# Performance work log

Hardware: AMD Instinct MI355X
Metric: run time of the kernel (lower is better)

The kernel has to match this reference:

```python
import jax, jax.numpy as jnp
from jax import lax
import numpy as np

ND1, ND2 = 48, 8   # stage_configs
LAMB = 1.5
EPS = 1e-12


def _make_proj(scale, n_views):
    H, W = 512 // scale, 640 // scale
    f = 700.0 / scale
    K = np.array([[f, 0, W / 2], [0, f, H / 2], [0, 0, 1]], np.float32)
    mats = []
    for v in range(n_views):
        a = 0.04 * v
        R = np.array([[np.cos(a), 0, np.sin(a)], [0, 1, 0], [-np.sin(a), 0, np.cos(a)]], np.float32)
        E = np.eye(4, dtype=np.float32)
        E[:3, :3] = R
        E[0, 3] = 20.0 * v
        Kin = np.eye(4, dtype=np.float32)
        Kin[:3, :3] = K
        mats.append(np.stack([E, Kin]))
    return jnp.asarray(np.stack(mats))[None]  # [1,V,2,4,4]


def setup_inputs():
    key = jax.random.key(0)
    ks = jax.random.split(key, 5)
    return {
        'feats1': jax.random.normal(ks[0], (1, 3, 32, 128, 160), jnp.float32),
        'feats2': jax.random.normal(ks[1], (1, 3, 16, 256, 320), jnp.float32),
        'proj1': _make_proj(4, 3),
        'proj2': _make_proj(2, 3),
        'depth_values': jnp.linspace(425.0, 935.0, ND1, dtype=jnp.float32)[None],
        'img': jax.random.normal(ks[2], (1, 3, 512, 640), jnp.float32),
        'w1': jax.random.normal(ks[3], (1, 32, 3, 3, 3), jnp.float32) * 0.05,
        'b1': jnp.zeros((1,), jnp.float32),
        'w2': jax.random.normal(ks[4], (1, 16, 3, 3, 3), jnp.float32) * 0.05,
        'b2': jnp.zeros((1,), jnp.float32),
    }


def _compose(p):
    # p: [B,2,4,4] -> K @ E[:3,:4] placed in top 3 rows of the extrinsic
    top = jnp.einsum('bij,bjk->bik', p[:, 1, :3, :3], p[:, 0, :3, :4])
    return p[:, 0].at[:, :3, :4].set(top)


def _bilinear(fea, x, y):
    # grid_sample(mode='bilinear', padding_mode='zeros', align_corners=False)
    # fea [B,C,H,W]; x,y pixel coords [B,P] -> [B,C,P]
    B, C, H, W = fea.shape
    flat = fea.reshape(B, C, H * W)
    x0, y0 = jnp.floor(x), jnp.floor(y)

    def gather(xi, yi):
        valid = (xi >= 0) & (xi <= W - 1) & (yi >= 0) & (yi <= H - 1)
        idx = (jnp.clip(yi, 0, H - 1) * W + jnp.clip(xi, 0, W - 1)).astype(jnp.int32)
        v = jnp.take_along_axis(flat, idx[:, None, :], axis=2)
        return jnp.where(valid[:, None, :], v, 0.0)

    wx, wy = x - x0, y - y0
    return (gather(x0, y0) * ((1 - wx) * (1 - wy))[:, None]
            + gather(x0 + 1, y0) * (wx * (1 - wy))[:, None]
            + gather(x0, y0 + 1) * ((1 - wx) * wy)[:, None]
            + gather(x0 + 1, y0 + 1) * (wx * wy)[:, None])


def _homo_warp(src_fea, src_proj, ref_proj, depth_samps):
    B, C, H, W = src_fea.shape
    D = depth_samps.shape[1]
    proj = jnp.einsum('bij,bjk->bik', src_proj, jnp.linalg.inv(ref_proj))
    rot, trans = proj[:, :3, :3], proj[:, :3, 3:4]
    yy, xx = jnp.meshgrid(jnp.arange(H, dtype=src_fea.dtype),
                          jnp.arange(W, dtype=src_fea.dtype), indexing='ij')
    xyz = jnp.stack([xx.ravel(), yy.ravel(), jnp.ones(H * W, src_fea.dtype)])  # [3,HW]
    rot_xyz = jnp.einsum('bij,jp->bip', rot, xyz)                               # [B,3,HW]
    pxyz = rot_xyz[:, :, None, :] * depth_samps.reshape(B, 1, D, -1) + trans[:, :, None, :]  # [B,3,D,HW]
    gx = pxyz[:, 0] / pxyz[:, 2] / ((W - 1) / 2) - 1.0
    gy = pxyz[:, 1] / pxyz[:, 2] / ((H - 1) / 2) - 1.0
    ix = ((gx + 1.0) * W - 1.0) / 2.0  # unnormalize, align_corners=False
    iy = ((gy + 1.0) * H - 1.0) / 2.0
    warped = _bilinear(src_fea, ix.reshape(B, -1), iy.reshape(B, -1))
    return warped.reshape(B, C, D, H, W)


def _conv3d(x, w, b):
    y = lax.conv_general_dilated(x, w, (1, 1, 1), 'SAME',
                                 dimension_numbers=('NCDHW', 'OIDHW', 'NCDHW'))
    return y + b.reshape(1, -1, 1, 1, 1)


def _stage(feats, projs, depth_samps, w, b):
    # feats [B,V,C,H,W], projs [B,V,2,4,4], depth_samps [B,D,H,W]
    B, V, C, H, W = feats.shape
    D = depth_samps.shape[1]
    ref_proj = _compose(projs[:, 0])
    ref_vol = jnp.broadcast_to(feats[:, 0][:, :, None], (B, C, D, H, W))
    vsum, vsq = ref_vol, ref_vol ** 2
    for v in range(1, V):  # small fixed number of views
        wv = _homo_warp(feats[:, v], _compose(projs[:, v]), ref_proj, depth_samps)
        vsum = vsum + wv
        vsq = vsq + wv ** 2
    variance = vsq / V - (vsum / V) ** 2
    prob = jax.nn.softmax(_conv3d(variance, w, b)[:, 0], axis=1)  # [B,D,H,W]
    depth = jnp.sum(prob * depth_samps, axis=1)                   # [B,H,W]
    p = jnp.pad(prob, ((0, 0), (1, 2), (0, 0), (0, 0)))
    sum4 = p[:, 0:D] + p[:, 1:D + 1] + p[:, 2:D + 2] + p[:, 3:D + 3]  # 4*avg_pool3d((4,1,1))
    di = jnp.sum(prob * jnp.arange(D, dtype=prob.dtype)[None, :, None, None], axis=1)
    di = jnp.clip(di.astype(jnp.int32), 0, D - 1)
    conf = jnp.take_along_axis(sum4, di[:, None], axis=1)[:, 0]
    exp_var = LAMB * jnp.sqrt(jnp.sum((depth_samps - depth[:, None]) ** 2 * prob, axis=1))
    return depth, conf, exp_var


def _forward(feats1, feats2, proj1, proj2, depth_values, img, w1, b1, w2, b2):
    B, _, Hi, Wi = img.shape
    H1, W1 = Hi // 4, Wi // 4
    H2, W2 = Hi // 2, Wi // 2
    # stage 1: depth_values is [B,D] -> uniform sampling path
    dmin, dmax = depth_values[:, 0], depth_values[:, -1]
    step1 = (dmax - dmin) / (ND1 - 1)
    s1 = dmin[:, None] + jnp.arange(ND1, dtype=jnp.float32)[None] * step1[:, None]
    samps1 = jnp.broadcast_to(s1[:, :, None, None], (B, ND1, H1, W1))
    d1, c1, v1 = _stage(feats1, proj1, samps1, w1, b1)
    # stage 2: detach + bilinear upsample + uncertainty-aware samples
    cur_d = jax.image.resize(lax.stop_gradient(d1)[:, None], (B, 1, H2, W2), 'bilinear')
    cur_v = jax.image.resize(lax.stop_gradient(v1)[:, None], (B, 1, H2, W2), 'bilinear')
    low = -jnp.minimum(cur_d, cur_v)
    step2 = (cur_v - low) / (ND2 - 1.0)
    samps2 = cur_d + low + step2 * jnp.arange(ND2, dtype=jnp.float32)[None, :, None, None] + EPS
    d2, c2, v2 = _stage(feats2, proj2, samps2, w2, b2)
    return (d1, c1, v1, d2, c2, v2)


def reference(feats1, feats2, proj1, proj2, depth_values, img, w1, b1, w2, b2):
    return _forward(feats1, feats2, proj1, proj2, depth_values, img, w1, b1, w2, b2)
```

## Files before the change

### kernel.cpp

```cpp
#include <hip/hip_runtime.h>
#include <math.h>


typedef _Float16 half2_t __attribute__((ext_vector_type(2)));
typedef _Float16 half8_t __attribute__((ext_vector_type(8)));

union U4H { uint4 u; half2_t h[4]; };
union U2H { uint2 u; half2_t h[2]; };

static __device__ inline float fdot2f(half2_t a, half2_t b, float c) {
#if __has_builtin(__builtin_amdgcn_fdot2)
  return __builtin_amdgcn_fdot2(a, b, c, false);
#else
  return c + (float)a[0] * (float)b[0] + (float)a[1] * (float)b[1];
#endif
}

__global__ void setup_mats_kernel(const float* __restrict__ proj1,
                                  const float* __restrict__ proj2,
                                  const float* __restrict__ depthv, int nd,
                                  float* __restrict__ ws,
                                  const float* __restrict__ w1,
                                  const float* __restrict__ w2,
                                  _Float16* __restrict__ w2a,
                                  _Float16* __restrict__ w2b) {
  const int tid = threadIdx.x;
  if (w2a != nullptr) {
    for (int i = tid; i < 27 * 32; i += 256) {
      int c = i % 32, r = i / 32, kd = r % 3, t = r / 3;
      w2a[(t * 3 + kd) * 32 + c] = (_Float16)w1[c * 27 + kd * 9 + t];
    }
    for (int i = tid; i < 27 * 16; i += 256) {
      int c = i % 16, r = i / 16, kd = r % 3, t = r / 3;
      w2b[(t * 3 + kd) * 16 + c] = (_Float16)w2[c * 27 + kd * 9 + t];
    }
  }
  if (tid != 0) return;
  for (int s = 0; s < 2; ++s) {
    const float* P = s ? proj2 : proj1;
    double comp[3][4][4];
    for (int v = 0; v < 3; ++v) {
      const float* E = P + v * 32;
      const float* K = P + v * 32 + 16;
      for (int r = 0; r < 3; ++r)
        for (int c = 0; c < 4; ++c) {
          double acc = 0.0;
          for (int k = 0; k < 3; ++k) acc += (double)K[r * 4 + k] * (double)E[k * 4 + c];
          comp[v][r][c] = acc;
        }
      for (int c = 0; c < 4; ++c) comp[v][3][c] = (double)E[12 + c];
    }
    double a[4][8];
    for (int r = 0; r < 4; ++r)
      for (int c = 0; c < 4; ++c) {
        a[r][c] = comp[0][r][c];
        a[r][4 + c] = (r == c) ? 1.0 : 0.0;
      }
    for (int col = 0; col < 4; ++col) {
      int piv = col;
      double best = fabs(a[col][col]);
      for (int r = col + 1; r < 4; ++r) {
        double t = fabs(a[r][col]);
        if (t > best) { best = t; piv = r; }
      }
      if (piv != col)
        for (int c = 0; c < 8; ++c) { double t = a[col][c]; a[col][c] = a[piv][c]; a[piv][c] = t; }
      double dv = a[col][col];
      for (int c = 0; c < 8; ++c) a[col][c] /= dv;
      for (int r = 0; r < 4; ++r)
        if (r != col) {
          double f = a[r][col];
          if (f != 0.0)
            for (int c = 0; c < 8; ++c) a[r][c] -= f * a[col][c];
        }
    }
    for (int v = 1; v < 3; ++v) {
      double Pm[3][4];
      for (int r = 0; r < 3; ++r)
        for (int c = 0; c < 4; ++c) {
          double acc = 0.0;
          for (int k = 0; k < 4; ++k) acc += comp[v][r][k] * a[k][4 + c];
          Pm[r][c] = acc;
        }
      float* o = ws + s * 24 + (v - 1) * 12;
      o[0] = (float)Pm[0][0]; o[1] = (float)Pm[0][1]; o[2] = (float)Pm[0][2];
      o[3] = (float)Pm[1][0]; o[4] = (float)Pm[1][1]; o[5] = (float)Pm[1][2];
      o[6] = (float)Pm[2][0]; o[7] = (float)Pm[2][1]; o[8] = (float)Pm[2][2];
      o[9] = (float)Pm[0][3]; o[10] = (float)Pm[1][3]; o[11] = (float)Pm[2][3];
    }
  }
  ws[48] = depthv[0];
  ws[49] = (depthv[nd - 1] - depthv[0]) / 47.0f;
}

template <int C, int H, int W>
__device__ inline void transpose_body(const float* __restrict__ in,
                                      _Float16* __restrict__ out,
                                      int x, int h, int v, float* s_t) {
  const int tid = threadIdx.x;
  const int w0 = x * 32;
  for (int r = tid; r < C * 32; r += 256) {
    int c = r >> 5, w = r & 31;
    s_t[c * 33 + w] = in[((size_t)(v * C + c) * H + h) * W + w0 + w];
  }
  __syncthreads();
  for (int r = tid; r < 32 * C; r += 256) {
    int w = r / C, c = r - (r / C) * C;
    out[((size_t)(v * H + h) * W + w0 + w) * C + c] = (_Float16)s_t[c * 33 + w];
  }
}

__global__ void transpose_both_kernel(const float* __restrict__ in1,
                                      _Float16* __restrict__ out1,
                                      const float* __restrict__ in2,
                                      _Float16* __restrict__ out2) {
  __shared__ float s_t[32 * 33];
  int bid = blockIdx.x;
  if (bid < 1920) {
    int x = bid % 5, h = (bid / 5) % 128, v = bid / (5 * 128);
    transpose_body<32, 128, 160>(in1, out1, x, h, v, s_t);
  } else {
    int b = bid - 1920;
    int x = b % 10, h = (b / 10) % 256, v = b / (10 * 256);
    transpose_body<16, 256, 320>(in2, out2, x, h, v, s_t);
  }
}

template <int D, int H, int W>
__device__ inline void stage2_range(const float* __restrict__ prev_d,
                                    const float* __restrict__ prev_v,
                                    int gy, int gx, float& base, float& st) {
  constexpr int SH = H / 2, SW = W / 2;
  float syf = 0.5f * (float)gy - 0.25f;
  float sxf = 0.5f * (float)gx - 0.25f;
  syf = fminf(fmaxf(syf, 0.0f), (float)(SH - 1));
  sxf = fminf(fmaxf(sxf, 0.0f), (float)(SW - 1));
  int sy0 = (int)syf, sx0 = (int)sxf;
  float fy2 = syf - (float)sy0, fx2 = sxf - (float)sx0;
  int sy1 = min(sy0 + 1, SH - 1), sx1 = min(sx0 + 1, SW - 1);
  int j00 = sy0 * SW + sx0, j01 = sy0 * SW + sx1;
  int j10 = sy1 * SW + sx0, j11 = sy1 * SW + sx1;
  float cd = (prev_d[j00] * (1.f - fx2) + prev_d[j01] * fx2) * (1.f - fy2) +
             (prev_d[j10] * (1.f - fx2) + prev_d[j11] * fx2) * fy2;
  float cv = (prev_v[j00] * (1.f - fx2) + prev_v[j01] * fx2) * (1.f - fy2) +
             (prev_v[j10] * (1.f - fx2) + prev_v[j11] * fx2) * fy2;
  float lo = -fminf(cd, cv);
  base = cd + lo + 1e-12f;
  st = (cv - lo) / (float)(D - 1);
}

template <int D, int H, int W>
__global__ void range_kernel(const float* __restrict__ prev_d,
                             const float* __restrict__ prev_v,
                             float2* __restrict__ rng) {
  int pix = blockIdx.x * 256 + threadIdx.x;
  if (pix >= H * W) return;
  float b, s;
  stage2_range<D, H, W>(prev_d, prev_v, pix / W, pix % W, b, s);
  rng[pix] = make_float2(b, s);
}

template <int C, int DTOT, int H, int W, bool STAGE2>
__launch_bounds__(256)
__global__ void gather_var_kernel(const _Float16* __restrict__ feats,
                                  const float* __restrict__ mats,
                                  const float* __restrict__ dpar,
                                  const float2* __restrict__ rng,
                                  _Float16* __restrict__ var_out) {
  constexpr int C8 = C / 8;
  const int idx = blockIdx.x * 256 + threadIdx.x;
  if (idx >= DTOT * H * W) return;
  const int gx = idx % W;
  const int t2 = idx / W;
  const int gy = t2 % H;
  const int d = t2 / H;
  const int pix = gy * W + gx;

  float base, st;
  if constexpr (STAGE2) {
    float2 r = rng[pix];
    base = r.x;
    st = r.y;
  } else {
    base = dpar[0];
    st = dpar[1];
  }
  const float dep = base + (float)d * st;

  const half8_t* fp = (const half8_t*)feats;
  float s[C], q[C];
#pragma unroll
  for (int cg = 0; cg < C8; ++cg) {
    half8_t r = fp[(size_t)pix * C8 + cg];
#pragma unroll
    for (int j = 0; j < 8; ++j) {
      float x = (float)r[j];
      s[cg * 8 + j] = x;
      q[cg * 8 + j] = x * x;
    }
  }

#pragma unroll
  for (int v = 0; v < 2; ++v) {
    const float* M = mats + v * 12;
    float fx = (float)gx, fy = (float)gy;
    float X = (M[0] * fx + M[1] * fy + M[2]) * dep + M[9];
    float Y = (M[3] * fx + M[4] * fy + M[5]) * dep + M[10];
    float Z = (M[6] * fx + M[7] * fy + M[8]) * dep + M[11];
    float inv = 1.0f / Z;
    float xz = X * inv, yz = Y * inv;
    float gxn = xz * (2.0f / (float)(W - 1)) - 1.0f;
    float gyn = yz * (2.0f / (float)(H - 1)) - 1.0f;
    float ix = ((gxn + 1.0f) * (float)W - 1.0f) * 0.5f;
    float iy = ((gyn + 1.0f) * (float)H - 1.0f) * 0.5f;
    float x0f = floorf(ix), y0f = floorf(iy);
    float wx = ix - x0f, wy = iy - y0f;
    float x1f = x0f + 1.0f, y1f = y0f + 1.0f;
    bool vx0 = (x0f >= 0.0f) && (x0f <= (float)(W - 1));
    bool vx1 = (x1f >= 0.0f) && (x1f <= (float)(W - 1));
    bool vy0 = (y0f >= 0.0f) && (y0f <= (float)(H - 1));
    bool vy1 = (y1f >= 0.0f) && (y1f <= (float)(H - 1));
    int xc0 = (int)fminf(fmaxf(x0f, 0.0f), (float)(W - 1));
    int xc1 = (int)fminf(fmaxf(x1f, 0.0f), (float)(W - 1));
    int yc0 = (int)fminf(fmaxf(y0f, 0.0f), (float)(H - 1));
    int yc1 = (int)fminf(fmaxf(y1f, 0.0f), (float)(H - 1));
    float wxm = 1.0f - wx, wym = 1.0f - wy;
    float a00 = (vx0 && vy0) ? wxm * wym : 0.0f;
    float a10 = (vx1 && vy0) ? wx * wym : 0.0f;
    float a01 = (vx0 && vy1) ? wxm * wy : 0.0f;
    float a11 = (vx1 && vy1) ? wx * wy : 0.0f;
    const size_t vb = (size_t)(v + 1) * H * W * C8;
    const size_t i00 = vb + (size_t)(yc0 * W + xc0) * C8;
    const size_t i10 = vb + (size_t)(yc0 * W + xc1) * C8;
    const size_t i01 = vb + (size_t)(yc1 * W + xc0) * C8;
    const size_t i11 = vb + (size_t)(yc1 * W + xc1) * C8;
#pragma unroll
    for (int cg = 0; cg < C8; ++cg) {
      half8_t p00 = fp[i00 + cg];
      half8_t p10 = fp[i10 + cg];
      half8_t p01 = fp[i01 + cg];
      half8_t p11 = fp[i11 + cg];
#pragma unroll
      for (int j = 0; j < 8; ++j) {
        float g = a00 * (float)p00[j] + a10 * (float)p10[j] +
                  a01 * (float)p01[j] + a11 * (float)p11[j];
        s[cg * 8 + j] += g;
        q[cg * 8 + j] += g * g;
      }
    }
  }
#pragma unroll
  for (int cg = 0; cg < C8; ++cg) {
    half8_t o;
#pragma unroll
    for (int j = 0; j < 8; ++j) {
      float m = s[cg * 8 + j] * (1.0f / 3.0f);
      o[j] = (_Float16)(q[cg * 8 + j] * (1.0f / 3.0f) - m * m);
    }
    *(half8_t*)(var_out + ((size_t)(d * C8 + cg) * (H * W) + pix) * 8) = o;
  }
}

template <int C, int DTOT, int DC, int H, int W, bool EPI>
__launch_bounds__(256)
__global__ void conv_cost_kernel(const uint4* __restrict__ var_in,
                                 const _Float16* __restrict__ w2h,
                                 const float* __restrict__ bconv,
                                 float* __restrict__ g_cost,
                                 const float2* __restrict__ rng,
                                 float* __restrict__ out_d,
                                 float* __restrict__ out_c,
                                 float* __restrict__ out_v) {
  constexpr int TH = 8, TW = 8, WB = 10, HALO = 100, NPX = 64;
  constexpr int NS = DC + 2;
  constexpr int CPG = C / 4;
  constexpr int HW = H * W;
  constexpr int C8 = C / 8;
  constexpr int REC = (CPG == 8) ? 16 : 8;

  __shared__ __align__(16) unsigned char s_wv_raw[4 * NS * HALO * REC];
  __shared__ __align__(16) unsigned char s_wt_raw[4 * 27 * REC];
  __shared__ float s_part[4 * DC * NPX];

  uint4* s_wv4 = (uint4*)s_wv_raw;
  uint2* s_wv2 = (uint2*)s_wv_raw;
  uint4* s_wt4 = (uint4*)s_wt_raw;
  uint2* s_wt2 = (uint2*)s_wt_raw;

  const int tid = threadIdx.x;
  const int lane = tid & 63;
  const int grp = tid >> 6;
  const int h0 = blockIdx.y * TH;
  const int w0 = blockIdx.x * TW;
  const int d0 = blockIdx.z * DC;

  if (lane < 27) {
    if constexpr (CPG == 8)
      s_wt4[grp * 27 + lane] = *(const uint4*)(w2h + lane * C + grp * CPG);
    else
      s_wt2[grp * 27 + lane] = *(const uint2*)(w2h + lane * C + grp * CPG);
  }

  int gidx[2], ldi[2];
  bool act[2], gval[2];
#pragma unroll
  for (int k = 0; k < 2; ++k) {
    int i = lane + k * 64;
    act[k] = (i < HALO);
    int hy = i / WB, hx = i - (i / WB) * WB;
    int gy = h0 + hy - 1, gx = w0 + hx - 1;
    gval[k] = act[k] && gy >= 0 && gy < H && gx >= 0 && gx < W;
    gidx[k] = gval[k] ? (gy * W + gx) : 0;
    ldi[k] = i;
  }

  if constexpr (CPG == 8) {
    uint4 pf[NS][2];
#pragma unroll
    for (int s = 0; s < NS; ++s) {
      int ds = d0 - 1 + s;
      bool dv = (ds >= 0) && (ds < DTOT);
#pragma unroll
      for (int k = 0; k < 2; ++k) {
        uint4 r = make_uint4(0u, 0u, 0u, 0u);
        if (dv && gval[k]) r = var_in[(size_t)(ds * C8 + grp) * HW + gidx[k]];
        pf[s][k] = r;
      }
    }
#pragma unroll
    for (int s = 0; s < NS; ++s)
#pragma unroll
      for (int k = 0; k < 2; ++k)
        if (act[k]) s_wv4[(grp * NS + s) * HALO + ldi[k]] = pf[s][k];
  } else {
    uint2 pf[NS][2];
#pragma unroll
    for (int s = 0; s < NS; ++s) {
      int ds = d0 - 1 + s;
      bool dv = (ds >= 0) && (ds < DTOT);
#pragma unroll
      for (int k = 0; k < 2; ++k) {
        uint2 r = make_uint2(0u, 0u);
        if (dv && gval[k])
          r = ((const uint2*)var_in)[((size_t)(ds * C8 + (grp >> 1)) * HW + gidx[k]) * 2 +
                                     (grp & 1)];
        pf[s][k] = r;
      }
    }
#pragma unroll
    for (int s = 0; s < NS; ++s)
#pragma unroll
      for (int k = 0; k < 2; ++k)
        if (act[k]) s_wv2[(grp * NS + s) * HALO + ldi[k]] = pf[s][k];
  }

  const int opx = lane;
  const int py = opx >> 3, pxx = opx & 7;

  float accA[NS], accB[NS], accC[NS];
#pragma unroll
  for (int s = 0; s < NS; ++s) { accA[s] = 0.f; accB[s] = 0.f; accC[s] = 0.f; }

#pragma unroll
  for (int t = 0; t < 9; ++t) {
    const int kh = t / 3, kw = t - 3 * kh;
    const int hp = (py + kh) * WB + (pxx + kw);
    if constexpr (CPG == 8) {
      U4H w0v, w1v, w2v;
      w0v.u = s_wt4[grp * 27 + t * 3 + 0];
      w1v.u = s_wt4[grp * 27 + t * 3 + 1];
      w2v.u = s_wt4[grp * 27 + t * 3 + 2];
#pragma unroll
      for (int s = 0; s < NS; ++s) {
        U4H v;
        v.u = s_wv4[(grp * NS + s) * HALO + hp];
        float a = 0.f, b = 0.f, c = 0.f;
#pragma unroll
        for (int j = 0; j < 4; ++j) {
          a = fdot2f(v.h[j], w0v.h[j], a);
          b = fdot2f(v.h[j], w1v.h[j], b);
          c = fdot2f(v.h[j], w2v.h[j], c);
        }
        accA[s] += a;
        accB[s] += b;
        accC[s] += c;
      }
    } else {
      U2H w0v, w1v, w2v;
      w0v.u = s_wt2[grp * 27 + t * 3 + 0];
      w1v.u = s_wt2[grp * 27 + t * 3 + 1];
      w2v.u = s_wt2[grp * 27 + t * 3 + 2];
#pragma unroll
      for (int s = 0; s < NS; ++s) {
        U2H v;
        v.u = s_wv2[(grp * NS + s) * HALO + hp];
        float a = 0.f, b = 0.f, c = 0.f;
#pragma unroll
        for (int j = 0; j < 2; ++j) {
          a = fdot2f(v.h[j], w0v.h[j], a);
          b = fdot2f(v.h[j], w1v.h[j], b);
          c = fdot2f(v.h[j], w2v.h[j], c);
        }
        accA[s] += a;
        accB[s] += b;
        accC[s] += c;
      }
    }
  }

#pragma unroll
  for (int j = 0; j < DC; ++j)
    s_part[grp * (DC * NPX) + j * NPX + opx] = accA[j] + accB[j + 1] + accC[j + 2];
  __syncthreads();

  const float bias = bconv[0];
  if constexpr (!EPI) {
    for (int i = tid; i < DC * NPX; i += 256) {
      float v = bias + s_part[i] + s_part[DC * NPX + i] + s_part[2 * DC * NPX + i] +
                s_part[3 * DC * NPX + i];
      int dd = i / NPX, o = i - dd * NPX;
      int oy = o / TW, ox = o - oy * TW;
      g_cost[(size_t)(d0 + dd) * (H * W) + (h0 + oy) * W + (w0 + ox)] = v;
    }
  } else {
    for (int i = tid; i < DC * NPX; i += 256)
      s_part[i] = bias + s_part[i] + s_part[DC * NPX + i] + s_part[2 * DC * NPX + i] +
                  s_part[3 * DC * NPX + i];
    __syncthreads();
    if (tid < NPX) {
      const int gy = h0 + py, gx = w0 + pxx;
      const int pix = gy * W + gx;
      float2 r = rng[pix];
      const float base = r.x, stp = r.y;
      float c[DC];
#pragma unroll
      for (int dd = 0; dd < DC; ++dd) c[dd] = s_part[dd * NPX + opx];
      float mx = -3.0e38f;
#pragma unroll
      for (int dd = 0; dd < DC; ++dd) mx = fmaxf(mx, c[dd]);
      float se = 0.f;
#pragma unroll
      for (int dd = 0; dd < DC; ++dd) {
        float e = expf(c[dd] - mx);
        c[dd] = e;
        se += e;
      }
      float depth = 0.f, dif = 0.f;
#pragma unroll
      for (int dd = 0; dd < DC; ++dd) {
        float p = c[dd] / se;
        c[dd] = p;
        depth += p * (base + (float)dd * stp);
        dif += p * (float)dd;
      }
      int di = (int)dif;
      di = min(max(di, 0), DC - 1);
      float conf = 0.f;
#pragma unroll
      for (int dd = 0; dd < DC; ++dd)
        if (dd >= di - 1 && dd <= di + 2) conf += c[dd];
      float ev = 0.f;
#pragma unroll
      for (int dd = 0; dd < DC; ++dd) {
        float sv = base + (float)dd * stp - depth;
        ev += sv * sv * c[dd];
      }
      ev = 1.5f * sqrtf(ev);
      out_d[pix] = depth;
      out_c[pix] = conf;
      out_v[pix] = ev;
    }
  }
}

template <int D, int H, int W, bool STAGE2>
__global__ void epilogue_kernel(const float* __restrict__ g_cost,
                                const float* __restrict__ dpar,
                                const float2* __restrict__ rng,
                                float* __restrict__ out_d,
                                float* __restrict__ out_c,
                                float* __restrict__ out_v) {
  int pix = blockIdx.x * 256 + threadIdx.x;
  if (pix >= H * W) return;
  float base, st;
  if constexpr (STAGE2) {
    float2 r = rng[pix];
    base = r.x;
    st = r.y;
  } else {
    base = dpar[0];
    st = dpar[1];
  }
  float c[D];
#pragma unroll
  for (int dd = 0; dd < D; ++dd) c[dd] = g_cost[(size_t)dd * (H * W) + pix];
  float mx = -3.0e38f;
#pragma unroll
  for (int dd = 0; dd < D; ++dd) mx = fmaxf(mx, c[dd]);
  float se = 0.f;
#pragma unroll
  for (int dd = 0; dd < D; ++dd) {
    float e = expf(c[dd] - mx);
    c[dd] = e;
    se += e;
  }
  float depth = 0.f, dif = 0.f;
#pragma unroll
  for (int dd = 0; dd < D; ++dd) {
    float p = c[dd] / se;
    c[dd] = p;
    depth += p * (base + (float)dd * st);
    dif += p * (float)dd;
  }
  int di = (int)dif;
  di = min(max(di, 0), D - 1);
  float conf = 0.f;
#pragma unroll
  for (int dd = 0; dd < D; ++dd)
    if (dd >= di - 1 && dd <= di + 2) conf += c[dd];
  float ev = 0.f;
#pragma unroll
  for (int dd = 0; dd < D; ++dd) {
    float sv = base + (float)dd * st - depth;
    ev += sv * sv * c[dd];
  }
  ev = 1.5f * sqrtf(ev);
  out_d[pix] = depth;
  out_c[pix] = conf;
  out_v[pix] = ev;
}


template <int C, int DTOT, int DC, int TH, int TW, int H, int W, bool STAGE2, bool EPI>
__launch_bounds__(256)
__global__ void cost_kernel(const float* __restrict__ feats,
                            const float* __restrict__ wconv,
                            const float* __restrict__ bconv,
                            const float* __restrict__ mats,
                            const float* __restrict__ dpar,
                            const float* __restrict__ prev_d,
                            const float* __restrict__ prev_v,
                            float* __restrict__ g_cost,
                            float* __restrict__ out_d,
                            float* __restrict__ out_c,
                            float* __restrict__ out_v) {
  constexpr int HB = TH + 2, WB = TW + 2, HALO = HB * WB, NPX = TH * TW;
  constexpr int HP = HALO + 1;
  constexpr int CG = C / 4;
  constexpr int NS = DC + 2;
  constexpr int VITEMS = HALO * C;

  __shared__ float s_var[2][C * HP];
  __shared__ float s_cost[DC * NPX];
  __shared__ float s_w[C * 27];
  __shared__ float s_rx[2][HALO], s_ry[2][HALO], s_rz[2][HALO];
  __shared__ float s_cw[2][2][4][HALO];
  __shared__ int s_ci[2][2][4][HALO];
  __shared__ int s_gidx[HALO];
  __shared__ float s_dbase[HALO], s_dstep[HALO];
  __shared__ unsigned char s_inb[HALO];

  const int tid = threadIdx.x;
  const int h0 = blockIdx.y * TH;
  const int w0 = blockIdx.x * TW;
  const int d0 = EPI ? 0 : blockIdx.z * DC;

  for (int i = tid; i < C * 27; i += 256) s_w[i] = wconv[i];

  for (int i = tid; i < HALO; i += 256) {
    int hy = i / WB, hx = i - hy * WB;
    int gy = h0 + hy - 1, gx = w0 + hx - 1;
    bool inb = (gy >= 0) && (gy < H) && (gx >= 0) && (gx < W);
    s_inb[i] = inb ? 1 : 0;
    s_gidx[i] = inb ? (gy * W + gx) : 0;
    float fx = (float)gx, fy = (float)gy;
#pragma unroll
    for (int v = 0; v < 2; ++v) {
      const float* M = mats + v * 12;
      s_rx[v][i] = M[0] * fx + M[1] * fy + M[2];
      s_ry[v][i] = M[3] * fx + M[4] * fy + M[5];
      s_rz[v][i] = M[6] * fx + M[7] * fy + M[8];
    }
    if constexpr (STAGE2) {
      float b, stp;
      stage2_range<DTOT, H, W>(prev_d, prev_v, gy, gx, b, stp);
      s_dbase[i] = b;
      s_dstep[i] = stp;
    } else {
      s_dbase[i] = dpar[0];
      s_dstep[i] = dpar[1];
    }
  }
  {
    float bias = bconv[0];
    for (int i = tid; i < DC * NPX; i += 256) s_cost[i] = bias;
  }
  __syncthreads();

  auto do_coords = [&](int ds, int b, int i) {
    int v = (i >= HALO) ? 1 : 0;
    int px = i - v * HALO;
    float dep = s_dbase[px] + (float)ds * s_dstep[px];
    const float* M = mats + v * 12;
    float X = s_rx[v][px] * dep + M[9];
    float Y = s_ry[v][px] * dep + M[10];
    float Z = s_rz[v][px] * dep + M[11];
    float inv = 1.0f / Z;
    float xz = X * inv, yz = Y * inv;
    float gxn = xz * (2.0f / (float)(W - 1)) - 1.0f;
    float gyn = yz * (2.0f / (float)(H - 1)) - 1.0f;
    float ix = ((gxn + 1.0f) * (float)W - 1.0f) * 0.5f;
    float iy = ((gyn + 1.0f) * (float)H - 1.0f) * 0.5f;
    float x0f = floorf(ix), y0f = floorf(iy);
    float wx = ix - x0f, wy = iy - y0f;
    float x1f = x0f + 1.0f, y1f = y0f + 1.0f;
    bool vx0 = (x0f >= 0.0f) && (x0f <= (float)(W - 1));
    bool vx1 = (x1f >= 0.0f) && (x1f <= (float)(W - 1));
    bool vy0 = (y0f >= 0.0f) && (y0f <= (float)(H - 1));
    bool vy1 = (y1f >= 0.0f) && (y1f <= (float)(H - 1));
    int xc0 = (int)fminf(fmaxf(x0f, 0.0f), (float)(W - 1));
    int xc1 = (int)fminf(fmaxf(x1f, 0.0f), (float)(W - 1));
    int yc0 = (int)fminf(fmaxf(y0f, 0.0f), (float)(H - 1));
    int yc1 = (int)fminf(fmaxf(y1f, 0.0f), (float)(H - 1));
    s_ci[b][v][0][px] = yc0 * W + xc0;
    s_ci[b][v][1][px] = yc0 * W + xc1;
    s_ci[b][v][2][px] = yc1 * W + xc0;
    s_ci[b][v][3][px] = yc1 * W + xc1;
    float wxm = 1.0f - wx, wym = 1.0f - wy;
    s_cw[b][v][0][px] = (vx0 && vy0) ? wxm * wym : 0.0f;
    s_cw[b][v][1][px] = (vx1 && vy0) ? wx * wym : 0.0f;
    s_cw[b][v][2][px] = (vx0 && vy1) ? wxm * wy : 0.0f;
    s_cw[b][v][3][px] = (vx1 && vy1) ? wx * wy : 0.0f;
  };

  auto do_variance = [&](int b, int b2, int i) {
    int c = i / HALO, px = i - (i / HALO) * HALO;
    float var = 0.f;
    if (s_inb[px]) {
      const float* f0 = feats + (size_t)c * (H * W);
      float rr = f0[s_gidx[px]];
      float sum = rr, ssq = rr * rr;
#pragma unroll
      for (int v = 0; v < 2; ++v) {
        const float* fv = feats + ((size_t)(v + 1) * C + c) * (H * W);
        float val = s_cw[b][v][0][px] * fv[s_ci[b][v][0][px]] +
                    s_cw[b][v][1][px] * fv[s_ci[b][v][1][px]] +
                    s_cw[b][v][2][px] * fv[s_ci[b][v][2][px]] +
                    s_cw[b][v][3][px] * fv[s_ci[b][v][3][px]];
        sum += val;
        ssq += val * val;
      }
      float m = sum / 3.0f;
      var = ssq / 3.0f - m * m;
    }
    s_var[b2][c * HP + px] = var;
  };

  auto conv_accum = [&](int ds, int sb) {
    for (int i = tid; i < NPX * 4; i += 256) {
      int grp = i / NPX, opx = i - grp * NPX;
      int py = opx / TW, pxx = opx - py * TW;
      float a0 = 0.f, a1 = 0.f, a2 = 0.f;
      int cbase = grp * CG;
#pragma unroll
      for (int kh = 0; kh < 3; ++kh) {
#pragma unroll
        for (int kw = 0; kw < 3; ++kw) {
          int hp = (py + kh) * WB + (pxx + kw);
#pragma unroll
          for (int cc = 0; cc < CG; ++cc) {
            int c = cbase + cc;
            float vv = s_var[sb][c * HP + hp];
            const float* wp = s_w + c * 27 + kh * 3 + kw;
            a0 += vv * wp[0];
            a1 += vv * wp[9];
            a2 += vv * wp[18];
          }
        }
      }
      int t0 = ds + 1 - d0;
      int t1 = ds - d0;
      int t2 = ds - 1 - d0;
      if (t0 >= 0 && t0 < DC) atomicAdd(&s_cost[t0 * NPX + opx], a0);
      if (t1 >= 0 && t1 < DC) atomicAdd(&s_cost[t1 * NPX + opx], a1);
      if (t2 >= 0 && t2 < DC) atomicAdd(&s_cost[t2 * NPX + opx], a2);
    }
  };

  {
    int ds0 = d0 - 1;
    if (ds0 >= 0 && ds0 < DTOT)
      for (int i = tid; i < 2 * HALO; i += 256) do_coords(ds0, 0, i);
  }
  __syncthreads();

  for (int s = 0; s <= NS; ++s) {
    const int ds = d0 - 1 + s;
    const bool val_cur = (s < NS) && (ds >= 0) && (ds < DTOT);
    const bool val_next = (s + 1 < NS) && (ds + 1 >= 0) && (ds + 1 < DTOT);
    const bool val_prev = (s >= 1) && (ds - 1 >= 0) && (ds - 1 < DTOT);
    if (val_cur)
      for (int i = tid; i < VITEMS; i += 256) do_variance(s & 1, s & 1, i);
    if (val_next)
      for (int i = tid; i < 2 * HALO; i += 256) do_coords(ds + 1, (s + 1) & 1, i);
    if (val_prev) conv_accum(ds - 1, (s - 1) & 1);
    __syncthreads();
  }

  if constexpr (!EPI) {
    for (int i = tid; i < DC * NPX; i += 256) {
      int dd = i / NPX, opx = i - dd * NPX;
      int py = opx / TW, pxx = opx - py * TW;
      g_cost[(size_t)(d0 + dd) * (H * W) + (h0 + py) * W + (w0 + pxx)] = s_cost[i];
    }
  } else if (tid < NPX) {
    const int opx = tid;
    const int py = opx / TW, pxx = opx - py * TW;
    const int hp = (py + 1) * WB + (pxx + 1);
    const float base = s_dbase[hp], st = s_dstep[hp];
    float mx = -3.0e38f;
    for (int dd = 0; dd < DTOT; ++dd) mx = fmaxf(mx, s_cost[dd * NPX + opx]);
    float se = 0.f;
    for (int dd = 0; dd < DTOT; ++dd) {
      float e = expf(s_cost[dd * NPX + opx] - mx);
      s_cost[dd * NPX + opx] = e;
      se += e;
    }
    float depth = 0.f, dif = 0.f;
    for (int dd = 0; dd < DTOT; ++dd) {
      float p = s_cost[dd * NPX + opx] / se;
      s_cost[dd * NPX + opx] = p;
      depth += p * (base + (float)dd * st);
      dif += p * (float)dd;
    }
    int di = (int)dif;
    di = min(max(di, 0), DTOT - 1);
    float conf = 0.f;
    for (int k = di - 1; k <= di + 2; ++k)
      if (k >= 0 && k < DTOT) conf += s_cost[k * NPX + opx];
    float ev = 0.f;
    for (int dd = 0; dd < DTOT; ++dd) {
      float sv = base + (float)dd * st - depth;
      ev += sv * sv * s_cost[dd * NPX + opx];
    }
    ev = 1.5f * sqrtf(ev);
    int gy = h0 + py, gx = w0 + pxx;
    out_d[gy * W + gx] = depth;
    out_c[gy * W + gx] = conf;
    out_v[gy * W + gx] = ev;
  }
}

extern "C" void kernel_launch(void* const* d_in, const int* in_sizes, int n_in,
                              void* d_out, int out_size, void* d_ws, size_t ws_size,
                              hipStream_t stream) {
  const float* feats1 = (const float*)d_in[0];
  const float* feats2 = (const float*)d_in[1];
  const float* proj1 = (const float*)d_in[2];
  const float* proj2 = (const float*)d_in[3];
  const float* depthv = (const float*)d_in[4];
  const float* w1 = (const float*)d_in[6];
  const float* b1 = (const float*)d_in[7];
  const float* w2 = (const float*)d_in[8];
  const float* b2 = (const float*)d_in[9];
  float* out = (float*)d_out;
  float* ws = (float*)d_ws;

  const int nd = in_sizes[4];
  const size_t F1 = (size_t)3 * 32 * 128 * 160;
  const size_t F2 = (size_t)3 * 16 * 256 * 320;
  const size_t COST1 = (size_t)48 * 128 * 160;
  const size_t COST2 = (size_t)8 * 256 * 320;
  const size_t VAR1 = (size_t)48 * 128 * 160 * 32;
  const size_t VAR2 = (size_t)8 * 256 * 320 * 16;
  const size_t RNG2 = (size_t)2 * 256 * 320;
  const size_t HDR = 1408;
  const size_t HUGE_FLOATS =
      HDR + COST1 + COST2 + F1 / 2 + F2 / 2 + VAR1 / 2 + VAR2 / 2 + RNG2;
  const bool huge = ws_size >= HUGE_FLOATS * sizeof(float);
  const bool mid = ws_size >= (64 + COST1) * sizeof(float);

  float* d1 = out;
  float* c1 = out + 20480;
  float* v1 = out + 40960;
  float* d2 = out + 61440;
  float* c2 = out + 143360;
  float* v2 = out + 225280;

  dim3 g1f(160 / 8, 128 / 8, 1), g2(320 / 8, 256 / 8, 1);

  if (huge) {
    _Float16* w2a = (_Float16*)(ws + 64);
    _Float16* w2b = (_Float16*)(ws + 512);
    float* cost1 = ws + HDR;
    float* cost2 = cost1 + COST1;
    _Float16* f1t = (_Float16*)(cost2 + COST2);
    _Float16* f2t = (_Float16*)(cost2 + COST2 + F1 / 2);
    _Float16* var1 = (_Float16*)(cost2 + COST2 + F1 / 2 + F2 / 2);
    _Float16* var2 = (_Float16*)(cost2 + COST2 + F1 / 2 + F2 / 2 + VAR1 / 2);
    float2* rng2 = (float2*)(cost2 + COST2 + F1 / 2 + F2 / 2 + VAR1 / 2 + VAR2 / 2);
    setup_mats_kernel<<<1, 256, 0, stream>>>(proj1, proj2, depthv, nd, ws, w1, w2, w2a, w2b);
    transpose_both_kernel<<<1920 + 7680, 256, 0, stream>>>(feats1, f1t, feats2, f2t);
    gather_var_kernel<32, 48, 128, 160, false>
        <<<(int)((48 * 128 * 160 + 255) / 256), 256, 0, stream>>>(f1t, ws, ws + 48, nullptr,
                                                                  var1);
    conv_cost_kernel<32, 48, 4, 128, 160, false><<<dim3(20, 16, 12), 256, 0, stream>>>(
        (const uint4*)var1, w2a, b1, cost1, nullptr, nullptr, nullptr, nullptr);
    epilogue_kernel<48, 128, 160, false><<<80, 256, 0, stream>>>(
        cost1, ws + 48, nullptr, d1, c1, v1);
    range_kernel<8, 256, 320><<<320, 256, 0, stream>>>(d1, v1, rng2);
    gather_var_kernel<16, 8, 256, 320, true>
        <<<(int)((8 * 256 * 320 + 255) / 256), 256, 0, stream>>>(f2t, ws + 24, ws + 48, rng2,
                                                                 var2);
    conv_cost_kernel<16, 8, 8, 256, 320, true><<<dim3(40, 32, 1), 256, 0, stream>>>(
        (const uint4*)var2, w2b, b2, nullptr, rng2, d2, c2, v2);
  } else if (mid) {
    float* cost1 = ws + 64;
    setup_mats_kernel<<<1, 256, 0, stream>>>(proj1, proj2, depthv, nd, ws, w1, w2,
                                             nullptr, nullptr);
    cost_kernel<32, 48, 8, 8, 8, 128, 160, false, false><<<dim3(20, 16, 6), 256, 0, stream>>>(
        feats1, w1, b1, ws, ws + 48, nullptr, nullptr, cost1, nullptr, nullptr, nullptr);
    epilogue_kernel<48, 128, 160, false><<<80, 256, 0, stream>>>(
        cost1, ws + 48, nullptr, d1, c1, v1);
    cost_kernel<16, 8, 8, 8, 8, 256, 320, true, true><<<g2, 256, 0, stream>>>(
        feats2, w2, b2, ws + 24, ws + 48, d1, v1, nullptr, d2, c2, v2);
  } else {
    setup_mats_kernel<<<1, 256, 0, stream>>>(proj1, proj2, depthv, nd, ws, w1, w2,
                                             nullptr, nullptr);
    cost_kernel<32, 48, 48, 8, 8, 128, 160, false, true><<<g1f, 256, 0, stream>>>(
        feats1, w1, b1, ws, ws + 48, nullptr, nullptr, nullptr, d1, c1, v1);
    cost_kernel<16, 8, 8, 8, 8, 256, 320, true, true><<<g2, 256, 0, stream>>>(
        feats2, w2, b2, ws + 24, ws + 48, d1, v1, nullptr, d2, c2, v2);
  }
}
```

Before: 224.7 us.

## Compute variance in packed fp16, loop depths per thread, inline stage-2 range

The gather/variance kernel now handles several depth hypotheses per thread (DPT=4), so the reference-view features and ray coefficients are loaded and computed once and reused across depths. The bilinear blending and sum/sum-of-squares accumulation move from fp32 to packed half8 arithmetic. The separate range_kernel is dropped and the stage-2 depth range is recomputed inline in both gather and conv kernels, which removes one launch and the rng buffer. Accumulating in fp16 risks precision loss in the variance (q/3 - m^2 cancellation), and having fewer threads reduces available parallelism.

Result: slower. 242.1 us (+7.7%).

```diff
diff --git a/kernel.cpp b/kernel.cpp
--- a/kernel.cpp
+++ b/kernel.cpp
@@ -149,115 +149,109 @@
   st = (cv - lo) / (float)(D - 1);
 }
 
-template <int D, int H, int W>
-__global__ void range_kernel(const float* __restrict__ prev_d,
-                             const float* __restrict__ prev_v,
-                             float2* __restrict__ rng) {
-  int pix = blockIdx.x * 256 + threadIdx.x;
-  if (pix >= H * W) return;
-  float b, s;
-  stage2_range<D, H, W>(prev_d, prev_v, pix / W, pix % W, b, s);
-  rng[pix] = make_float2(b, s);
-}
-
-template <int C, int DTOT, int H, int W, bool STAGE2>
+template <int C, int DTOT, int DPT, int H, int W, bool STAGE2>
 __launch_bounds__(256)
 __global__ void gather_var_kernel(const _Float16* __restrict__ feats,
                                   const float* __restrict__ mats,
                                   const float* __restrict__ dpar,
-                                  const float2* __restrict__ rng,
+                                  const float* __restrict__ prev_d,
+                                  const float* __restrict__ prev_v,
                                   _Float16* __restrict__ var_out) {
   constexpr int C8 = C / 8;
+  constexpr int NB = DTOT / DPT;
   const int idx = blockIdx.x * 256 + threadIdx.x;
-  if (idx >= DTOT * H * W) return;
+  if (idx >= NB * H * W) return;
   const int gx = idx % W;
   const int t2 = idx / W;
   const int gy = t2 % H;
-  const int d = t2 / H;
+  const int db = t2 / H;
   const int pix = gy * W + gx;
 
   float base, st;
   if constexpr (STAGE2) {
-    float2 r = rng[pix];
-    base = r.x;
-    st = r.y;
+    stage2_range<DTOT, H, W>(prev_d, prev_v, gy, gx, base, st);
   } else {
     base = dpar[0];
     st = dpar[1];
   }
-  const float dep = base + (float)d * st;
 
   const half8_t* fp = (const half8_t*)feats;
-  float s[C], q[C];
+  half8_t rh[C8], rq[C8];
 #pragma unroll
   for (int cg = 0; cg < C8; ++cg) {
-    half8_t r = fp[(size_t)pix * C8 + cg];
-#pragma unroll
-    for (int j = 0; j < 8; ++j) {
-      float x = (float)r[j];
-      s[cg * 8 + j] = x;
-      q[cg * 8 + j] = x * x;
-    }
-  }
-
-#pragma unroll
-  for (int v = 0; v < 2; ++v) {
-    const float* M = mats + v * 12;
-    float fx = (float)gx, fy = (float)gy;
-    float X = (M[0] * fx + M[1] * fy + M[2]) * dep + M[9];
-    float Y = (M[3] * fx + M[4] * fy + M[5]) * dep + M[10];
-    float Z = (M[6] * fx + M[7] * fy + M[8]) * dep + M[11];
-    float inv = 1.0f / Z;
-    float xz = X * inv, yz = Y * inv;
-    float gxn = xz * (2.0f / (float)(W - 1)) - 1.0f;
-    float gyn = yz * (2.0f / (float)(H - 1)) - 1.0f;
-    float ix = ((gxn + 1.0f) * (float)W - 1.0f) * 0.5f;
-    float iy = ((gyn + 1.0f) * (float)H - 1.0f) * 0.5f;
-    float x0f = floorf(ix), y0f = floorf(iy);
-    float wx = ix - x0f, wy = iy - y0f;
-    float x1f = x0f + 1.0f, y1f = y0f + 1.0f;
-    bool vx0 = (x0f >= 0.0f) && (x0f <= (float)(W - 1));
-    bool vx1 = (x1f >= 0.0f) && (x1f <= (float)(W - 1));
-    bool vy0 = (y0f >= 0.0f) && (y0f <= (float)(H - 1));
-    bool vy1 = (y1f >= 0.0f) && (y1f <= (float)(H - 1));
-    int xc0 = (int)fminf(fmaxf(x0f, 0.0f), (float)(W - 1));
-    int xc1 = (int)fminf(fmaxf(x1f, 0.0f), (float)(W - 1));
-    int yc0 = (int)fminf(fmaxf(y0f, 0.0f), (float)(H - 1));
-    int yc1 = (int)fminf(fmaxf(y1f, 0.0f), (float)(H - 1));
-    float wxm = 1.0f - wx, wym = 1.0f - wy;
-    float a00 = (vx0 && vy0) ? wxm * wym : 0.0f;
-    float a10 = (vx1 && vy0) ? wx * wym : 0.0f;
-    float a01 = (vx0 && vy1) ? wxm * wy : 0.0f;
-    float a11 = (vx1 && vy1) ? wx * wy : 0.0f;
-    const size_t vb = (size_t)(v + 1) * H * W * C8;
-    const size_t i00 = vb + (size_t)(yc0 * W + xc0) * C8;
-    const size_t i10 = vb + (size_t)(yc0 * W + xc1) * C8;
-    const size_t i01 = vb + (size_t)(yc1 * W + xc0) * C8;
-    const size_t i11 = vb + (size_t)(yc1 * W + xc1) * C8;
+    rh[cg] = fp[(size_t)pix * C8 + cg];
+    rq[cg] = rh[cg] * rh[cg];
+  }
+
+  float rx[2], ry[2], rz[2];
+  {
+    const float fx = (float)gx, fy = (float)gy;
+#pragma unroll
+    for (int v = 0; v < 2; ++v) {
+      const float* M = mats + v * 12;
+      rx[v] = M[0] * fx + M[1] * fy + M[2];
+      ry[v] = M[3] * fx + M[4] * fy + M[5];
+      rz[v] = M[6] * fx + M[7] * fy + M[8];
+    }
+  }
+
+  const _Float16 third = (_Float16)(1.0f / 3.0f);
+  for (int dd = 0; dd < DPT; ++dd) {
+    const int d = db * DPT + dd;
+    const float dep = base + (float)d * st;
+    half8_t sa[C8], qa[C8];
 #pragma unroll
     for (int cg = 0; cg < C8; ++cg) {
-      half8_t p00 = fp[i00 + cg];
-      half8_t p10 = fp[i10 + cg];
-      half8_t p01 = fp[i01 + cg];
-      half8_t p11 = fp[i11 + cg];
-#pragma unroll
-      for (int j = 0; j < 8; ++j) {
-        float g = a00 * (float)p00[j] + a10 * (float)p10[j] +
-                  a01 * (float)p01[j] + a11 * (float)p11[j];
-        s[cg * 8 + j] += g;
-        q[cg * 8 + j] += g * g;
-      }
-    }
-  }
-#pragma unroll
-  for (int cg = 0; cg < C8; ++cg) {
-    half8_t o;
-#pragma unroll
-    for (int j = 0; j < 8; ++j) {
-      float m = s[cg * 8 + j] * (1.0f / 3.0f);
-      o[j] = (_Float16)(q[cg * 8 + j] * (1.0f / 3.0f) - m * m);
-    }
-    *(half8_t*)(var_out + ((size_t)(d * C8 + cg) * (H * W) + pix) * 8) = o;
+      sa[cg] = rh[cg];
+      qa[cg] = rq[cg];
+    }
+#pragma unroll
+    for (int v = 0; v < 2; ++v) {
+      const float* M = mats + v * 12;
+      float X = rx[v] * dep + M[9];
+      float Y = ry[v] * dep + M[10];
+      float Z = rz[v] * dep + M[11];
+      float inv = 1.0f / Z;
+      float xz = X * inv, yz = Y * inv;
+      float gxn = xz * (2.0f / (float)(W - 1)) - 1.0f;
+      float gyn = yz * (2.0f / (float)(H - 1)) - 1.0f;
+      float ix = ((gxn + 1.0f) * (float)W - 1.0f) * 0.5f;
+      float iy = ((gyn + 1.0f) * (float)H - 1.0f) * 0.5f;
+      float x0f = floorf(ix), y0f = floorf(iy);
+      float wx = ix - x0f, wy = iy - y0f;
+      float x1f = x0f + 1.0f, y1f = y0f + 1.0f;
+      bool vx0 = (x0f >= 0.0f) && (x0f <= (float)(W - 1));
+      bool vx1 = (x1f >= 0.0f) && (x1f <= (float)(W - 1));
+      bool vy0 = (y0f >= 0.0f) && (y0f <= (float)(H - 1));
+      bool vy1 = (y1f >= 0.0f) && (y1f <= (float)(H - 1));
+      int xc0 = (int)fminf(fmaxf(x0f, 0.0f), (float)(W - 1));
+      int xc1 = (int)fminf(fmaxf(x1f, 0.0f), (float)(W - 1));
+      int yc0 = (int)fminf(fmaxf(y0f, 0.0f), (float)(H - 1));
+      int yc1 = (int)fminf(fmaxf(y1f, 0.0f), (float)(H - 1));
+      float wxm = 1.0f - wx, wym = 1.0f - wy;
+      _Float16 h00 = (_Float16)((vx0 && vy0) ? wxm * wym : 0.0f);
+      _Float16 h10 = (_Float16)((vx1 && vy0) ? wx * wym : 0.0f);
+      _Float16 h01 = (_Float16)((vx0 && vy1) ? wxm * wy : 0.0f);
+      _Float16 h11 = (_Float16)((vx1 && vy1) ? wx * wy : 0.0f);
+      const size_t vb = (size_t)(v + 1) * H * W * C8;
+      const size_t i00 = vb + (size_t)(yc0 * W + xc0) * C8;
+      const size_t i10 = vb + (size_t)(yc0 * W + xc1) * C8;
+      const size_t i01 = vb + (size_t)(yc1 * W + xc0) * C8;
+      const size_t i11 = vb + (size_t)(yc1 * W + xc1) * C8;
+#pragma unroll
+      for (int cg = 0; cg < C8; ++cg) {
+        half8_t g = fp[i00 + cg] * h00 + fp[i10 + cg] * h10 +
+                    fp[i01 + cg] * h01 + fp[i11 + cg] * h11;
+        sa[cg] += g;
+        qa[cg] += g * g;
+      }
+    }
+#pragma unroll
+    for (int cg = 0; cg < C8; ++cg) {
+      half8_t m = sa[cg] * third;
+      half8_t o = qa[cg] * third - m * m;
+      *(half8_t*)(var_out + ((size_t)(d * C8 + cg) * (H * W) + pix) * 8) = o;
+    }
   }
 }
 
@@ -267,7 +261,8 @@
                                  const _Float16* __restrict__ w2h,
                                  const float* __restrict__ bconv,
                                  float* __restrict__ g_cost,
-                                 const float2* __restrict__ rng,
+                                 const float* __restrict__ prev_d,
+                                 const float* __restrict__ prev_v,
                                  float* __restrict__ out_d,
                                  float* __restrict__ out_c,
                                  float* __restrict__ out_v) {
@@ -430,8 +425,8 @@
     if (tid < NPX) {
       const int gy = h0 + py, gx = w0 + pxx;
       const int pix = gy * W + gx;
-      float2 r = rng[pix];
-      const float base = r.x, stp = r.y;
+      float base, stp;
+      stage2_range<DC, H, W>(prev_d, prev_v, gy, gx, base, stp);
       float c[DC];
 #pragma unroll
       for (int dd = 0; dd < DC; ++dd) c[dd] = s_part[dd * NPX + opx];
@@ -473,24 +468,15 @@
   }
 }
 
-template <int D, int H, int W, bool STAGE2>
+template <int D, int H, int W>
 __global__ void epilogue_kernel(const float* __restrict__ g_cost,
                                 const float* __restrict__ dpar,
-                                const float2* __restrict__ rng,
                                 float* __restrict__ out_d,
                                 float* __restrict__ out_c,
                                 float* __restrict__ out_v) {
   int pix = blockIdx.x * 256 + threadIdx.x;
   if (pix >= H * W) return;
-  float base, st;
-  if constexpr (STAGE2) {
-    float2 r = rng[pix];
-    base = r.x;
-    st = r.y;
-  } else {
-    base = dpar[0];
-    st = dpar[1];
-  }
+  const float base = dpar[0], st = dpar[1];
   float c[D];
 #pragma unroll
   for (int dd = 0; dd < D; ++dd) c[dd] = g_cost[(size_t)dd * (H * W) + pix];
@@ -798,30 +784,26 @@
     _Float16* f2t = (_Float16*)(cost2 + COST2 + F1 / 2);
     _Float16* var1 = (_Float16*)(cost2 + COST2 + F1 / 2 + F2 / 2);
     _Float16* var2 = (_Float16*)(cost2 + COST2 + F1 / 2 + F2 / 2 + VAR1 / 2);
-    float2* rng2 = (float2*)(cost2 + COST2 + F1 / 2 + F2 / 2 + VAR1 / 2 + VAR2 / 2);
     setup_mats_kernel<<<1, 256, 0, stream>>>(proj1, proj2, depthv, nd, ws, w1, w2, w2a, w2b);
     transpose_both_kernel<<<1920 + 7680, 256, 0, stream>>>(feats1, f1t, feats2, f2t);
-    gather_var_kernel<32, 48, 128, 160, false>
-        <<<(int)((48 * 128 * 160 + 255) / 256), 256, 0, stream>>>(f1t, ws, ws + 48, nullptr,
-                                                                  var1);
+    gather_var_kernel<32, 48, 4, 128, 160, false>
+        <<<(int)((12 * 128 * 160 + 255) / 256), 256, 0, stream>>>(f1t, ws, ws + 48, nullptr,
+                                                                  nullptr, var1);
     conv_cost_kernel<32, 48, 4, 128, 160, false><<<dim3(20, 16, 12), 256, 0, stream>>>(
-        (const uint4*)var1, w2a, b1, cost1, nullptr, nullptr, nullptr, nullptr);
-    epilogue_kernel<48, 128, 160, false><<<80, 256, 0, stream>>>(
-        cost1, ws + 48, nullptr, d1, c1, v1);
-    range_kernel<8, 256, 320><<<320, 256, 0, stream>>>(d1, v1, rng2);
-    gather_var_kernel<16, 8, 256, 320, true>
-        <<<(int)((8 * 256 * 320 + 255) / 256), 256, 0, stream>>>(f2t, ws + 24, ws + 48, rng2,
+        (const uint4*)var1, w2a, b1, cost1, nullptr, nullptr, nullptr, nullptr, nullptr);
+    epilogue_kernel<48, 128, 160><<<80, 256, 0, stream>>>(cost1, ws + 48, d1, c1, v1);
+    gather_var_kernel<16, 8, 4, 256, 320, true>
+        <<<(int)((2 * 256 * 320 + 255) / 256), 256, 0, stream>>>(f2t, ws + 24, ws + 48, d1, v1,
                                                                  var2);
     conv_cost_kernel<16, 8, 8, 256, 320, true><<<dim3(40, 32, 1), 256, 0, stream>>>(
-        (const uint4*)var2, w2b, b2, nullptr, rng2, d2, c2, v2);
+        (const uint4*)var2, w2b, b2, nullptr, d1, v1, d2, c2, v2);
   } else if (mid) {
     float* cost1 = ws + 64;
     setup_mats_kernel<<<1, 256, 0, stream>>>(proj1, proj2, depthv, nd, ws, w1, w2,
                                              nullptr, nullptr);
     cost_kernel<32, 48, 8, 8, 8, 128, 160, false, false><<<dim3(20, 16, 6), 256, 0, stream>>>(
         feats1, w1, b1, ws, ws + 48, nullptr, nullptr, cost1, nullptr, nullptr, nullptr);
-    epilogue_kernel<48, 128, 160, false><<<80, 256, 0, stream>>>(
-        cost1, ws + 48, nullptr, d1, c1, v1);
+    epilogue_kernel<48, 128, 160><<<80, 256, 0, stream>>>(cost1, ws + 48, d1, c1, v1);
     cost_kernel<16, 8, 8, 8, 8, 256, 320, true, true><<<g2, 256, 0, stream>>>(
         feats2, w2, b2, ws + 24, ws + 48, d1, v1, nullptr, d2, c2, v2);
   } else {
```
